# Performance work log

Hardware: AMD Instinct MI355X
Metric: run time of the kernel (lower is better)

The kernel has to match this reference:

```python
import jax, jax.numpy as jnp
import numpy as np

N_NODES = 100000
N_EDGES = 3200000
HID = 52
N_LAYERS = 3


def setup_inputs() -> dict:
    key = jax.random.key(0)
    ks = jax.random.split(key, 6)
    x = jax.random.normal(ks[0], (N_NODES, HID), dtype=jnp.float32)
    edge_index = jax.random.randint(ks[1], (2, N_EDGES), 0, N_NODES, dtype=jnp.int32)
    w1 = jax.random.normal(ks[2], (N_LAYERS, HID, 2 * HID), dtype=jnp.float32) * 0.1
    b1 = jnp.zeros((N_LAYERS, 2 * HID), dtype=jnp.float32)
    w2 = jax.random.normal(ks[3], (N_LAYERS, 2 * HID, HID), dtype=jnp.float32) * 0.1
    b2 = jnp.zeros((N_LAYERS, HID), dtype=jnp.float32)
    eps = jnp.zeros((N_LAYERS,), dtype=jnp.float32)
    lin_w = jax.random.normal(ks[4], (HID * (N_LAYERS + 1), HID), dtype=jnp.float32) * 0.1
    lin_b = jnp.zeros((HID,), dtype=jnp.float32)
    return {"x": x, "edge_index": edge_index, "w1": w1, "b1": b1,
            "w2": w2, "b2": b2, "eps": eps, "lin_w": lin_w, "lin_b": lin_b}


def reference(x, edge_index, w1, b1, w2, b2, eps, lin_w, lin_b):
    src, dst = edge_index[0], edge_index[1]
    n = x.shape[0]
    h = x
    h_list = [x]
    for l in range(N_LAYERS):
        # GINConv: sum-aggregate neighbor features at target nodes
        agg = jax.ops.segment_sum(h[src], dst, num_segments=n)  # [N, HID]
        z = (1.0 + eps[l]) * h + agg
        # 2-layer MLP: Linear -> ReLU -> Linear
        z = jnp.maximum(z @ w1[l] + b1[l], 0.0) @ w2[l] + b2[l]
        # outer ReLU (dropout p=0 is identity)
        h = jnp.maximum(z, 0.0)
        h_list.append(h)
    node_repr = jnp.concatenate(h_list, axis=1)  # [N, HID*(L+1)]
    return node_repr @ lin_w + lin_b
```

## Files before the change

### kernel.cpp

```cpp
#include <hip/hip_runtime.h>

#define HID 52
#define HID2 104
#define P1_CHUNK 8192
#define NBIN_MAX 512
#define HSTRIDE 136

typedef unsigned short ushort_t;
typedef unsigned int uint_t;
typedef short bf16x8 __attribute__((ext_vector_type(8)));
typedef float f32x4 __attribute__((ext_vector_type(4)));
typedef float f32x2 __attribute__((ext_vector_type(2)));

__device__ __forceinline__ ushort_t f2bf(float f) {
    union { float f; uint_t u; } c; c.f = f;
    uint_t u = c.u + 0x7FFFu + ((c.u >> 16) & 1u);
    return (ushort_t)(u >> 16);
}
__device__ __forceinline__ float bflo(uint_t u) {
    union { uint_t u; float f; } c; c.u = u << 16; return c.f;
}
__device__ __forceinline__ float bfhi(uint_t u) {
    union { uint_t u; float f; } c; c.u = u & 0xFFFF0000u; return c.f;
}
__device__ __forceinline__ f32x2 unpk2(uint_t u) {
    union { uint_t u; float f; } lo, hi;
    lo.u = u << 16; hi.u = u;
    return (f32x2){lo.f, hi.f};
}
__device__ __forceinline__ f32x2 rawpair(uint_t a, uint_t b) {
    union { uint_t u; float f; } ca, cb; ca.u = a; cb.u = b;
    return (f32x2){ca.f, cb.f};
}
__device__ __forceinline__ f32x2 shlpair(uint_t a, uint_t b) {
    union { uint_t u; float f; } ca, cb; ca.u = a << 16; cb.u = b << 16;
    return (f32x2){ca.f, cb.f};
}
__device__ __forceinline__ void pkacc(f32x2& a, f32x2 b) {
    asm("v_pk_add_f32 %0, %0, %1" : "+v"(a) : "v"(b));
}
__device__ __forceinline__ f32x2 shfl2(f32x2 v, int m) {
    f32x2 r;
    r.x = __shfl_xor(v.x, m);
    r.y = __shfl_xor(v.y, m);
    return r;
}

__global__ __launch_bounds__(256) void setup_kernel(const float* __restrict__ x,
                                                    const float* __restrict__ w1,
                                                    const float* __restrict__ w2,
                                                    const float* __restrict__ lin_w,
                                                    const int* __restrict__ dst,
                                                    ushort_t* __restrict__ xb,
                                                    ushort_t* __restrict__ h1b,
                                                    ushort_t* __restrict__ h2b,
                                                    ushort_t* __restrict__ w1f,
                                                    ushort_t* __restrict__ w2f,
                                                    ushort_t* __restrict__ linf,
                                                    int* __restrict__ ghist,
                                                    int n, int E, int nxblk) {
    __shared__ int lh[NBIN_MAX];
    int blk = blockIdx.x;
    int tid = threadIdx.x;
    if (blk < nxblk) {
        int t = blk * 256 + tid;
        if (t >= n * 16) return;
        int node = t >> 4, pp = t & 15;
        int c0 = pp * 4;
        ushort_t o[4];
#pragma unroll
        for (int j = 0; j < 4; j++) {
            int c = c0 + j;
            o[j] = (c < HID) ? f2bf(x[(size_t)node * HID + c]) : 0;
        }
        uint_t u0 = (uint_t)o[0] | ((uint_t)o[1] << 16);
        uint_t u1 = (uint_t)o[2] | ((uint_t)o[3] << 16);
        *(uint2*)(xb + (size_t)node * 64 + c0) = make_uint2(u0, u1);
        return;
    }
    if (blk == nxblk) {
        ushort_t* arr = (tid < 64) ? xb : (tid < 128) ? h1b : h2b;
        arr[(size_t)n * 64 + (tid & 63)] = 0;
        return;
    }
    if (blk < nxblk + 32) {
        int gid = (blk - nxblk - 1) * 4 + (tid >> 6);
        int lane = tid & 63;
        if (gid >= 122) return;
        int m = lane & 15, q = lane >> 4;
        ushort_t o[8];
        ushort_t* dstp;
        if (gid < 42) {
            int l = gid / 14, r = gid % 14, ct = r >> 1, ks = r & 1;
            int nn = ct * 16 + m;
#pragma unroll
            for (int j = 0; j < 8; j++) {
                int k = ks * 32 + q * 8 + j;
                o[j] = (k < HID && nn < HID2) ? f2bf(w1[((size_t)l * HID + k) * HID2 + nn]) : 0;
            }
            dstp = w1f + ((size_t)(l * 14 + ct * 2 + ks) * 64 + lane) * 8;
        } else if (gid < 90) {
            int g2 = gid - 42, l = g2 / 16, r = g2 % 16, ct = r >> 2, ks = r & 3;
            int nn = ct * 16 + m;
#pragma unroll
            for (int j = 0; j < 8; j++) {
                int k = ks * 32 + q * 8 + j;
                o[j] = (k < HID2 && nn < HID) ? f2bf(w2[((size_t)l * HID2 + k) * HID + nn]) : 0;
            }
            dstp = w2f + ((size_t)(l * 16 + ct * 4 + ks) * 64 + lane) * 8;
        } else {
            int g2 = gid - 90, ct = g2 >> 3, ks = g2 & 7;
            int nn = ct * 16 + m;
#pragma unroll
            for (int j = 0; j < 8; j++) {
                int kg = ks * 32 + q * 8 + j;
                int seg = kg >> 6, kk = kg & 63;
                o[j] = (kk < HID && nn < HID) ? f2bf(lin_w[((size_t)seg * HID + kk) * HID + nn]) : 0;
            }
            dstp = linf + ((size_t)(ct * 8 + ks) * 64 + lane) * 8;
        }
        uint4 u;
        u.x = (uint_t)o[0] | ((uint_t)o[1] << 16);
        u.y = (uint_t)o[2] | ((uint_t)o[3] << 16);
        u.z = (uint_t)o[4] | ((uint_t)o[5] << 16);
        u.w = (uint_t)o[6] | ((uint_t)o[7] << 16);
        *(uint4*)dstp = u;
        return;
    }
    int eblk = blk - nxblk - 32;
    lh[tid] = 0; lh[tid + 256] = 0;
    __syncthreads();
    int base = eblk * P1_CHUNK;
    int cend = min(P1_CHUNK, E - base);
    for (int i = tid; i < cend; i += 256) atomicAdd(&lh[dst[base + i] >> 8], 1);
    __syncthreads();
    int cc = lh[tid];       if (cc) atomicAdd(&ghist[tid], cc);
    cc = lh[tid + 256];     if (cc) atomicAdd(&ghist[tid + 256], cc);
}

__global__ __launch_bounds__(256) void pass1_kernel(const int* __restrict__ src,
                                                    const int* __restrict__ dst,
                                                    const int* __restrict__ ghist,
                                                    int* __restrict__ gcnt,
                                                    uint_t* __restrict__ packed, int E) {
    __shared__ uint_t stage[P1_CHUNK];
    __shared__ ushort_t sbin[P1_CHUNK];
    __shared__ int gh[NBIN_MAX];
    __shared__ int cnt[NBIN_MAX];
    __shared__ int sst[NBIN_MAX];
    __shared__ int curs[NBIN_MAX];
    __shared__ int gbase[NBIN_MAX];
    __shared__ int ps[256];
    int tid = threadIdx.x;
    int b0 = 2 * tid, b1 = 2 * tid + 1;
    gh[b0] = ghist[b0]; gh[b1] = ghist[b1];
    cnt[tid] = 0; cnt[tid + 256] = 0;
    __syncthreads();
    int gpair = gh[b0] + gh[b1];
    ps[tid] = gpair;
    __syncthreads();
    for (int off = 1; off < 256; off <<= 1) {
        int t = (tid >= off) ? ps[tid - off] : 0;
        __syncthreads();
        ps[tid] += t;
        __syncthreads();
    }
    int bst0 = ps[tid] - gpair;
    int bst1 = bst0 + gh[b0];
    __syncthreads();
    int base = blockIdx.x * P1_CHUNK;
    int cend = min(P1_CHUNK, E - base);
    for (int i = tid; i < cend; i += 256) atomicAdd(&cnt[dst[base + i] >> 8], 1);
    __syncthreads();
    int c0 = cnt[b0], c1 = cnt[b1];
    int pair = c0 + c1;
    ps[tid] = pair;
    __syncthreads();
    for (int off = 1; off < 256; off <<= 1) {
        int t = (tid >= off) ? ps[tid - off] : 0;
        __syncthreads();
        ps[tid] += t;
        __syncthreads();
    }
    int ex = ps[tid] - pair;
    sst[b0] = ex;       curs[b0] = ex;
    sst[b1] = ex + c0;  curs[b1] = ex + c0;
    gbase[b0] = c0 ? (bst0 + atomicAdd(&gcnt[b0], c0)) : 0;
    gbase[b1] = c1 ? (bst1 + atomicAdd(&gcnt[b1], c1)) : 0;
    __syncthreads();
    for (int i = tid; i < cend; i += 256) {
        int d = dst[base + i];
        int s = src[base + i];
        int b = d >> 8;
        int pos = atomicAdd(&curs[b], 1);
        stage[pos] = ((uint_t)s << 8) | (uint_t)(d & 255);
        sbin[pos] = (ushort_t)b;
    }
    __syncthreads();
    for (int i = tid; i < cend; i += 256) {
        int b = sbin[i];
        packed[gbase[b] + (i - sst[b])] = stage[i];
    }
}

__global__ __launch_bounds__(256) void pass2_kernel(const uint_t* __restrict__ packed,
                                                    const int* __restrict__ ghist,
                                                    int* __restrict__ srcsorted,
                                                    int* __restrict__ nrs,
                                                    int* __restrict__ ndeg, int N) {
    __shared__ int c[NBIN_MAX];
    __shared__ int ps[256];
    __shared__ int hist[256];
    __shared__ int curs[256];
    int b = blockIdx.x;
    int tid = threadIdx.x;
    int b0 = 2 * tid, b1 = 2 * tid + 1;
    int g0 = ghist[b0], g1 = ghist[b1];
    hist[tid] = 0;
    int gpair = g0 + g1;
    ps[tid] = gpair;
    __syncthreads();
    for (int off = 1; off < 256; off <<= 1) {
        int t = (tid >= off) ? ps[tid - off] : 0;
        __syncthreads();
        ps[tid] += t;
        __syncthreads();
    }
    int ex = ps[tid] - gpair;
    c[b0] = ex;
    c[b1] = ex + g0;
    __syncthreads();
    int beg = c[b];
    int end = beg + ghist[b];
    int obase = beg + b * 4096;
    for (int i = beg + tid; i < end; i += 256) atomicAdd(&hist[packed[i] & 255u], 1);
    __syncthreads();
    int v = hist[tid];
    int pv = (v + 15) & ~15;
    ps[tid] = pv;
    __syncthreads();
    for (int off = 1; off < 256; off <<= 1) {
        int t = (tid >= off) ? ps[tid - off] : 0;
        __syncthreads();
        ps[tid] += t;
        __syncthreads();
    }
    int start = obase + ps[tid] - pv;
    int node = b * 256 + tid;
    if (node < N) { nrs[node] = start; ndeg[node] = pv; }
    curs[tid] = start;
    __syncthreads();
    for (int i = beg + tid; i < end; i += 256) {
        uint_t p = packed[i];
        int pos = atomicAdd(&curs[p & 255u], 1);
        srcsorted[pos] = (int)(p >> 8);
    }
    __syncthreads();
    for (int i = start + v; i < start + pv; i++) srcsorted[i] = N;
}

__global__ __launch_bounds__(256) void agg_kernel(const ushort_t* __restrict__ hb,
                                                  const int* __restrict__ nrs,
                                                  const int* __restrict__ ndeg,
                                                  const int* __restrict__ srcsorted,
                                                  const float* __restrict__ eps,
                                                  ushort_t* __restrict__ zb, int n) {
    int wid = (blockIdx.x * blockDim.x + threadIdx.x) >> 6;
    if (wid >= n) return;
    int lane = threadIdx.x & 63;
    int g = lane >> 3, sub = lane & 7;
    int beg = nrs[wid];
    int total = ndeg[wid];
    const char* hc = (const char*)hb;
    const char* sp = (const char*)srcsorted;
    unsigned lbB = (unsigned)sub * 16u;
    unsigned sB = (unsigned)(beg + g) * 4u;

    f32x2 AO0 = {0,0}, AO1 = {0,0}, AE0 = {0,0}, AE1 = {0,0};
    f32x2 BO0 = {0,0}, BO1 = {0,0}, BE0 = {0,0}, BE1 = {0,0};
    if (total > 0) {
        unsigned bo = sB;
        int f0  = *(const int*)(sp + bo);
        int f1  = *(const int*)(sp + bo + 32);
        int f2r = *(const int*)(sp + bo + 64);
        int f3r = *(const int*)(sp + bo + 96);
        for (int b = 0; b < total; b += 32) {
            bool ok = (b + 16) < total;
            int e0 = f0, e1 = f1;
            int e2 = ok ? f2r : n;
            int e3 = ok ? f3r : n;
            f0  = *(const int*)(sp + bo + 128);
            f1  = *(const int*)(sp + bo + 160);
            f2r = *(const int*)(sp + bo + 192);
            f3r = *(const int*)(sp + bo + 224);
            bo += 128;
            uint4 v0 = *(const uint4*)(hc + (((unsigned)e0 << 7) + lbB));
            uint4 v1 = *(const uint4*)(hc + (((unsigned)e1 << 7) + lbB));
            uint4 v2 = *(const uint4*)(hc + (((unsigned)e2 << 7) + lbB));
            uint4 v3 = *(const uint4*)(hc + (((unsigned)e3 << 7) + lbB));
            pkacc(AO0, rawpair(v0.x, v0.y)); pkacc(AO1, rawpair(v0.z, v0.w));
            pkacc(AE0, shlpair(v0.x, v0.y)); pkacc(AE1, shlpair(v0.z, v0.w));
            pkacc(BO0, rawpair(v1.x, v1.y)); pkacc(BO1, rawpair(v1.z, v1.w));
            pkacc(BE0, shlpair(v1.x, v1.y)); pkacc(BE1, shlpair(v1.z, v1.w));
            pkacc(AO0, rawpair(v2.x, v2.y)); pkacc(AO1, rawpair(v2.z, v2.w));
            pkacc(AE0, shlpair(v2.x, v2.y)); pkacc(AE1, shlpair(v2.z, v2.w));
            pkacc(BO0, rawpair(v3.x, v3.y)); pkacc(BO1, rawpair(v3.z, v3.w));
            pkacc(BE0, shlpair(v3.x, v3.y)); pkacc(BE1, shlpair(v3.z, v3.w));
        }
    }
    pkacc(AO0, BO0); pkacc(AO1, BO1);
    pkacc(AE0, BE0); pkacc(AE1, BE1);
#pragma unroll
    for (int msk = 8; msk <= 32; msk <<= 1) {
        pkacc(AO0, shfl2(AO0, msk));
        pkacc(AO1, shfl2(AO1, msk));
        pkacc(AE0, shfl2(AE0, msk));
        pkacc(AE1, shfl2(AE1, msk));
    }
    if (lane < 8) {
        float sc = 1.0f + eps[0];
        uint4 sv = *(const uint4*)(hb + (size_t)wid * 64 + lane * 8);
        float o0 = fmaf(sc, bflo(sv.x), AE0.x), o1 = fmaf(sc, bfhi(sv.x), AO0.x);
        float o2 = fmaf(sc, bflo(sv.y), AE0.y), o3 = fmaf(sc, bfhi(sv.y), AO0.y);
        float o4 = fmaf(sc, bflo(sv.z), AE1.x), o5 = fmaf(sc, bfhi(sv.z), AO1.x);
        float o6 = fmaf(sc, bflo(sv.w), AE1.y), o7 = fmaf(sc, bfhi(sv.w), AO1.y);
        uint4 u;
        u.x = (uint_t)f2bf(o0) | ((uint_t)f2bf(o1) << 16);
        u.y = (uint_t)f2bf(o2) | ((uint_t)f2bf(o3) << 16);
        u.z = (uint_t)f2bf(o4) | ((uint_t)f2bf(o5) << 16);
        u.w = (uint_t)f2bf(o6) | ((uint_t)f2bf(o7) << 16);
        *(uint4*)(zb + (size_t)wid * 64 + lane * 8) = u;
    }
}

template<int LAST>
__global__ __launch_bounds__(256) void mlp_kernel(const ushort_t* __restrict__ zb,
                                                  const ushort_t* __restrict__ w1f,
                                                  const float* __restrict__ b1,
                                                  const ushort_t* __restrict__ w2f,
                                                  const float* __restrict__ b2,
                                                  ushort_t* __restrict__ hbout,
                                                  const ushort_t* __restrict__ xb,
                                                  const ushort_t* __restrict__ h1b,
                                                  const ushort_t* __restrict__ h2b,
                                                  const ushort_t* __restrict__ linf,
                                                  const float* __restrict__ lin_b,
                                                  float* __restrict__ out, int n) {
    __shared__ ushort_t hid[64 * HSTRIDE];
    __shared__ ushort_t h3t[LAST ? 64 * 68 : 1];
    int tid = threadIdx.x;
    int w = tid >> 6, lane = tid & 63, m = lane & 15, q = lane >> 4;
    for (int i = tid; i < 64 * 32; i += 256) {
        int r = i >> 5, c = HID2 + (i & 31);
        hid[r * HSTRIDE + c] = 0;
    }
    __syncthreads();

    int nb = blockIdx.x * 64 + w * 16;
    f32x4 acc1[7];
#pragma unroll
    for (int ct = 0; ct < 7; ct++) {
        int col = ct * 16 + m;
        float bv = (col < HID2) ? b1[col] : 0.f;
        acc1[ct] = (f32x4){bv, bv, bv, bv};
    }
    int anode = min(nb + m, n - 1);
#pragma unroll
    for (int ks = 0; ks < 2; ks++) {
        bf16x8 a = *(const bf16x8*)(zb + (size_t)anode * 64 + ks * 32 + q * 8);
#pragma unroll
        for (int ct = 0; ct < 7; ct++) {
            bf16x8 b = *(const bf16x8*)(w1f + ((size_t)(ct * 2 + ks) * 64 + lane) * 8);
            acc1[ct] = __builtin_amdgcn_mfma_f32_16x16x32_bf16(a, b, acc1[ct], 0, 0, 0);
        }
    }
#pragma unroll
    for (int ct = 0; ct < 7; ct++) {
#pragma unroll
        for (int r = 0; r < 4; r++) {
            float v = fmaxf(acc1[ct][r], 0.f);
            int row = w * 16 + q * 4 + r;
            hid[row * HSTRIDE + ct * 16 + m] = f2bf(v);
        }
    }
    f32x4 acc2[4];
#pragma unroll
    for (int ct = 0; ct < 4; ct++) {
        int col = ct * 16 + m;
        float bv = (col < HID) ? b2[col] : 0.f;
        acc2[ct] = (f32x4){bv, bv, bv, bv};
    }
#pragma unroll
    for (int ks = 0; ks < 4; ks++) {
        bf16x8 a = *(const bf16x8*)&hid[(w * 16 + m) * HSTRIDE + ks * 32 + q * 8];
#pragma unroll
        for (int ct = 0; ct < 4; ct++) {
            bf16x8 b = *(const bf16x8*)(w2f + ((size_t)(ct * 4 + ks) * 64 + lane) * 8);
            acc2[ct] = __builtin_amdgcn_mfma_f32_16x16x32_bf16(a, b, acc2[ct], 0, 0, 0);
        }
    }

    if (!LAST) {
#pragma unroll
        for (int ct = 0; ct < 4; ct++) {
#pragma unroll
            for (int r = 0; r < 4; r++) {
                int node = nb + q * 4 + r;
                if (node < n) {
                    float v = fmaxf(acc2[ct][r], 0.f);
                    hbout[(size_t)node * 64 + ct * 16 + m] = f2bf(v);
                }
            }
        }
    } else {
#pragma unroll
        for (int ct = 0; ct < 4; ct++) {
#pragma unroll
            for (int r = 0; r < 4; r++) {
                float v = fmaxf(acc2[ct][r], 0.f);
                h3t[(w * 16 + q * 4 + r) * 68 + ct * 16 + m] = f2bf(v);
            }
        }
        f32x4 accF[4];
#pragma unroll
        for (int ct = 0; ct < 4; ct++) {
            int col = ct * 16 + m;
            float bv = (col < HID) ? lin_b[col] : 0.f;
            accF[ct] = (f32x4){bv, bv, bv, bv};
        }
        const ushort_t* segs[3] = {xb, h1b, h2b};
#pragma unroll
        for (int ks = 0; ks < 8; ks++) {
            bf16x8 a;
            if (ks < 6) {
                const ushort_t* p = segs[ks >> 1];
                a = *(const bf16x8*)(p + (size_t)anode * 64 + (ks & 1) * 32 + q * 8);
            } else {
                a = *(const bf16x8*)&h3t[(w * 16 + m) * 68 + (ks & 1) * 32 + q * 8];
            }
#pragma unroll
            for (int ct = 0; ct < 4; ct++) {
                bf16x8 b = *(const bf16x8*)(linf + ((size_t)(ct * 8 + ks) * 64 + lane) * 8);
                accF[ct] = __builtin_amdgcn_mfma_f32_16x16x32_bf16(a, b, accF[ct], 0, 0, 0);
            }
        }
#pragma unroll
        for (int ct = 0; ct < 4; ct++) {
            int col = ct * 16 + m;
            if (col < HID) {
#pragma unroll
                for (int r = 0; r < 4; r++) {
                    int node = nb + q * 4 + r;
                    if (node < n)
                        out[(size_t)node * HID + col] = accF[ct][r];
                }
            }
        }
    }
}

extern "C" void kernel_launch(void* const* d_in, const int* in_sizes, int n_in,
                              void* d_out, int out_size, void* d_ws, size_t ws_size,
                              hipStream_t stream) {
    const float* x     = (const float*)d_in[0];
    const int*   ei    = (const int*)d_in[1];
    const float* w1    = (const float*)d_in[2];
    const float* b1    = (const float*)d_in[3];
    const float* w2    = (const float*)d_in[4];
    const float* b2    = (const float*)d_in[5];
    const float* eps   = (const float*)d_in[6];
    const float* lin_w = (const float*)d_in[7];
    const float* lin_b = (const float*)d_in[8];
    float* out = (float*)d_out;

    const int N = in_sizes[0] / HID;
    const int E = in_sizes[1] / 2;
    const int* src = ei;
    const int* dst = ei + E;

    const int NBIN = (N + 255) / 256;

    char* p = (char*)d_ws;
    const size_t ROWS = (size_t)(N + 1) * 64 * 2;
    ushort_t* xb  = (ushort_t*)p;  p += ROWS;
    ushort_t* zb  = (ushort_t*)p;  p += ROWS;
    ushort_t* h1b = (ushort_t*)p;  p += ROWS;
    ushort_t* h2b = (ushort_t*)p;  p += ROWS;
    ushort_t* w1f = (ushort_t*)p;  p += 3 * 14 * 512 * 2;
    ushort_t* w2f = (ushort_t*)p;  p += 3 * 16 * 512 * 2;
    ushort_t* linf= (ushort_t*)p;  p += 32 * 512 * 2;
    int* ghist    = (int*)p;       p += 512 * 4;
    int* gcnt     = (int*)p;       p += 512 * 4;
    int* nrs      = (int*)p;       p += (size_t)(N + 4) * 4;
    int* ndeg     = (int*)p;       p += (size_t)(N + 4) * 4;
    uint_t* packed = (uint_t*)p;   p += (size_t)E * 4;
    int* srcsorted = (int*)p;

    ushort_t* hbs[3] = {xb, h1b, h2b};

    const int BLK = 256;
    const int NP1 = (E + P1_CHUNK - 1) / P1_CHUNK;
    const int NXBLK = (N * 16 + BLK - 1) / BLK;
    const int NBUCK = (N + 63) / 64;
    dim3 blk(BLK);
    dim3 grid_agg(((size_t)N * 64 + BLK - 1) / BLK);

    hipMemsetAsync(ghist, 0, 1024 * sizeof(int), stream);
    setup_kernel<<<NXBLK + 32 + NP1, blk, 0, stream>>>(x, w1, w2, lin_w, dst,
                                                       xb, h1b, h2b,
                                                       w1f, w2f, linf, ghist, N, E, NXBLK);
    pass1_kernel<<<NP1, blk, 0, stream>>>(src, dst, ghist, gcnt, packed, E);
    pass2_kernel<<<NBIN, blk, 0, stream>>>(packed, ghist, srcsorted, nrs, ndeg, N);

    for (int l = 0; l < 2; l++) {
        agg_kernel<<<grid_agg, blk, 0, stream>>>(hbs[l], nrs, ndeg, srcsorted, eps + l, zb, N);
        mlp_kernel<0><<<NBUCK, blk, 0, stream>>>(zb,
                                                 w1f + (size_t)l * 14 * 512,
                                                 b1 + (size_t)l * HID2,
                                                 w2f + (size_t)l * 16 * 512,
                                                 b2 + (size_t)l * HID,
                                                 hbs[l + 1],
                                                 nullptr, nullptr, nullptr,
                                                 nullptr, nullptr, nullptr, N);
    }
    agg_kernel<<<grid_agg, blk, 0, stream>>>(h2b, nrs, ndeg, srcsorted, eps + 2, zb, N);
    mlp_kernel<1><<<NBUCK, blk, 0, stream>>>(zb,
                                             w1f + 2 * 14 * 512,
                                             b1 + 2 * HID2,
                                             w2f + 2 * 16 * 512,
                                             b2 + 2 * HID,
                                             nullptr,
                                             xb, h1b, h2b,
                                             linf, lin_b, out, N);
}
```

Measured before the change: 399.0 us.

## Process two nodes per wavefront in aggregation with swizzle reductions

The aggregation kernel now assigns one node to each 32-lane half of a wavefront instead of a full wavefront per node, so every lane group walks more edges per iteration (8 gathers unrolled instead of 4). The cross-group reduction switches from __shfl_xor across 64 lanes to ds_swizzle within 32 lanes. The aim is to halve the wasted lanes and the reduction overhead for low-degree nodes (average degree 32), at the cost of longer per-lane loops and more registers in flight.

Measured after the change: 391.0 us. 2.0% less time.

```diff
diff --git a/kernel.cpp b/kernel.cpp
--- a/kernel.cpp
+++ b/kernel.cpp
@@ -23,11 +23,6 @@
 __device__ __forceinline__ float bfhi(uint_t u) {
     union { uint_t u; float f; } c; c.u = u & 0xFFFF0000u; return c.f;
 }
-__device__ __forceinline__ f32x2 unpk2(uint_t u) {
-    union { uint_t u; float f; } lo, hi;
-    lo.u = u << 16; hi.u = u;
-    return (f32x2){lo.f, hi.f};
-}
 __device__ __forceinline__ f32x2 rawpair(uint_t a, uint_t b) {
     union { uint_t u; float f; } ca, cb; ca.u = a; cb.u = b;
     return (f32x2){ca.f, cb.f};
@@ -39,11 +34,13 @@
 __device__ __forceinline__ void pkacc(f32x2& a, f32x2 b) {
     asm("v_pk_add_f32 %0, %0, %1" : "+v"(a) : "v"(b));
 }
-__device__ __forceinline__ f32x2 shfl2(f32x2 v, int m) {
-    f32x2 r;
-    r.x = __shfl_xor(v.x, m);
-    r.y = __shfl_xor(v.y, m);
-    return r;
+template<int IMM>
+__device__ __forceinline__ f32x2 swz2(f32x2 v) {
+    union { float f; int i; } a, b; a.f = v.x; b.f = v.y;
+    int ra = __builtin_amdgcn_ds_swizzle(a.i, IMM);
+    int rb = __builtin_amdgcn_ds_swizzle(b.i, IMM);
+    union { int i; float f; } c, d; c.i = ra; d.i = rb;
+    return (f32x2){c.f, d.f};
 }
 
 __global__ __launch_bounds__(256) void setup_kernel(const float* __restrict__ x,
@@ -265,39 +262,55 @@
                                                   const int* __restrict__ srcsorted,
                                                   const float* __restrict__ eps,
                                                   ushort_t* __restrict__ zb, int n) {
-    int wid = (blockIdx.x * blockDim.x + threadIdx.x) >> 6;
-    if (wid >= n) return;
+    int wpair = (blockIdx.x * blockDim.x + threadIdx.x) >> 6;
     int lane = threadIdx.x & 63;
-    int g = lane >> 3, sub = lane & 7;
-    int beg = nrs[wid];
-    int total = ndeg[wid];
+    int half = lane >> 5;
+    int wid = wpair * 2 + half;
+    bool valid = (wid < n);
+    int node = valid ? wid : (n - 1);
+    int hl = lane & 31;
+    int g = hl >> 3;
+    int sub = lane & 7;
+    int beg = nrs[node];
+    int total = valid ? ndeg[node] : 0;
     const char* hc = (const char*)hb;
     const char* sp = (const char*)srcsorted;
     unsigned lbB = (unsigned)sub * 16u;
-    unsigned sB = (unsigned)(beg + g) * 4u;
+    unsigned bo = (unsigned)(beg + g) * 4u;
 
     f32x2 AO0 = {0,0}, AO1 = {0,0}, AE0 = {0,0}, AE1 = {0,0};
     f32x2 BO0 = {0,0}, BO1 = {0,0}, BE0 = {0,0}, BE1 = {0,0};
     if (total > 0) {
-        unsigned bo = sB;
-        int f0  = *(const int*)(sp + bo);
-        int f1  = *(const int*)(sp + bo + 32);
-        int f2r = *(const int*)(sp + bo + 64);
-        int f3r = *(const int*)(sp + bo + 96);
+        int f0 = *(const int*)(sp + bo);
+        int f1 = *(const int*)(sp + bo + 16);
+        int f2 = *(const int*)(sp + bo + 32);
+        int f3 = *(const int*)(sp + bo + 48);
+        int f4 = *(const int*)(sp + bo + 64);
+        int f5 = *(const int*)(sp + bo + 80);
+        int f6 = *(const int*)(sp + bo + 96);
+        int f7 = *(const int*)(sp + bo + 112);
         for (int b = 0; b < total; b += 32) {
             bool ok = (b + 16) < total;
-            int e0 = f0, e1 = f1;
-            int e2 = ok ? f2r : n;
-            int e3 = ok ? f3r : n;
-            f0  = *(const int*)(sp + bo + 128);
-            f1  = *(const int*)(sp + bo + 160);
-            f2r = *(const int*)(sp + bo + 192);
-            f3r = *(const int*)(sp + bo + 224);
+            int e0 = f0, e1 = f1, e2 = f2, e3 = f3;
+            int e4 = ok ? f4 : n, e5 = ok ? f5 : n;
+            int e6 = ok ? f6 : n, e7 = ok ? f7 : n;
+            f0 = *(const int*)(sp + bo + 128);
+            f1 = *(const int*)(sp + bo + 144);
+            f2 = *(const int*)(sp + bo + 160);
+            f3 = *(const int*)(sp + bo + 176);
+            f4 = *(const int*)(sp + bo + 192);
+            f5 = *(const int*)(sp + bo + 208);
+            f6 = *(const int*)(sp + bo + 224);
+            f7 = *(const int*)(sp + bo + 240);
             bo += 128;
             uint4 v0 = *(const uint4*)(hc + (((unsigned)e0 << 7) + lbB));
             uint4 v1 = *(const uint4*)(hc + (((unsigned)e1 << 7) + lbB));
             uint4 v2 = *(const uint4*)(hc + (((unsigned)e2 << 7) + lbB));
             uint4 v3 = *(const uint4*)(hc + (((unsigned)e3 << 7) + lbB));
+            uint4 v4 = *(const uint4*)(hc + (((unsigned)e4 << 7) + lbB));
+            uint4 v5 = *(const uint4*)(hc + (((unsigned)e5 << 7) + lbB));
+            uint4 v6 = *(const uint4*)(hc + (((unsigned)e6 << 7) + lbB));
+            uint4 v7 = *(const uint4*)(hc + (((unsigned)e7 << 7) + lbB));
             pkacc(AO0, rawpair(v0.x, v0.y)); pkacc(AO1, rawpair(v0.z, v0.w));
             pkacc(AE0, shlpair(v0.x, v0.y)); pkacc(AE1, shlpair(v0.z, v0.w));
             pkacc(BO0, rawpair(v1.x, v1.y)); pkacc(BO1, rawpair(v1.z, v1.w));
@@ -306,20 +319,25 @@
             pkacc(AE0, shlpair(v2.x, v2.y)); pkacc(AE1, shlpair(v2.z, v2.w));
             pkacc(BO0, rawpair(v3.x, v3.y)); pkacc(BO1, rawpair(v3.z, v3.w));
             pkacc(BE0, shlpair(v3.x, v3.y)); pkacc(BE1, shlpair(v3.z, v3.w));
+            pkacc(AO0, rawpair(v4.x, v4.y)); pkacc(AO1, rawpair(v4.z, v4.w));
+            pkacc(AE0, shlpair(v4.x, v4.y)); pkacc(AE1, shlpair(v4.z, v4.w));
+            pkacc(BO0, rawpair(v5.x, v5.y)); pkacc(BO1, rawpair(v5.z, v5.w));
+            pkacc(BE0, shlpair(v5.x, v5.y)); pkacc(BE1, shlpair(v5.z, v5.w));
+            pkacc(AO0, rawpair(v6.x, v6.y)); pkacc(AO1, rawpair(v6.z, v6.w));
+            pkacc(AE0, shlpair(v6.x, v6.y)); pkacc(AE1, shlpair(v6.z, v6.w));
+            pkacc(BO0, rawpair(v7.x, v7.y)); pkacc(BO1, rawpair(v7.z, v7.w));
+            pkacc(BE0, shlpair(v7.x, v7.y)); pkacc(BE1, shlpair(v7.z, v7.w));
         }
     }
     pkacc(AO0, BO0); pkacc(AO1, BO1);
     pkacc(AE0, BE0); pkacc(AE1, BE1);
-#pragma unroll
-    for (int msk = 8; msk <= 32; msk <<= 1) {
-        pkacc(AO0, shfl2(AO0, msk));
-        pkacc(AO1, shfl2(AO1, msk));
-        pkacc(AE0, shfl2(AE0, msk));
-        pkacc(AE1, shfl2(AE1, msk));
-    }
-    if (lane < 8) {
+    pkacc(AO0, swz2<0x201F>(AO0)); pkacc(AO1, swz2<0x201F>(AO1));
+    pkacc(AE0, swz2<0x201F>(AE0)); pkacc(AE1, swz2<0x201F>(AE1));
+    pkacc(AO0, swz2<0x401F>(AO0)); pkacc(AO1, swz2<0x401F>(AO1));
+    pkacc(AE0, swz2<0x401F>(AE0)); pkacc(AE1, swz2<0x401F>(AE1));
+    if (hl < 8 && valid) {
         float sc = 1.0f + eps[0];
-        uint4 sv = *(const uint4*)(hb + (size_t)wid * 64 + lane * 8);
+        uint4 sv = *(const uint4*)(hb + (size_t)wid * 64 + hl * 8);
         float o0 = fmaf(sc, bflo(sv.x), AE0.x), o1 = fmaf(sc, bfhi(sv.x), AO0.x);
         float o2 = fmaf(sc, bflo(sv.y), AE0.y), o3 = fmaf(sc, bfhi(sv.y), AO0.y);
         float o4 = fmaf(sc, bflo(sv.z), AE1.x), o5 = fmaf(sc, bfhi(sv.z), AO1.x);
@@ -329,7 +347,7 @@
         u.y = (uint_t)f2bf(o2) | ((uint_t)f2bf(o3) << 16);
         u.z = (uint_t)f2bf(o4) | ((uint_t)f2bf(o5) << 16);
         u.w = (uint_t)f2bf(o6) | ((uint_t)f2bf(o7) << 16);
-        *(uint4*)(zb + (size_t)wid * 64 + lane * 8) = u;
+        *(uint4*)(zb + (size_t)wid * 64 + hl * 8) = u;
     }
 }
 
@@ -502,8 +520,9 @@
     const int NP1 = (E + P1_CHUNK - 1) / P1_CHUNK;
     const int NXBLK = (N * 16 + BLK - 1) / BLK;
     const int NBUCK = (N + 63) / 64;
+    const int NPAIR = (N + 1) / 2;
     dim3 blk(BLK);
-    dim3 grid_agg(((size_t)N * 64 + BLK - 1) / BLK);
+    dim3 grid_agg(((size_t)NPAIR * 64 + BLK - 1) / BLK);
 
     hipMemsetAsync(ghist, 0, 1024 * sizeof(int), stream);
     setup_kernel<<<NXBLK + 32 + NP1, blk, 0, stream>>>(x, w1, w2, lin_w, dst,
```
